# Kernel tuning notes

Hardware: AMD Instinct MI355X
Metric: run time of the kernel (lower is better)

## Reference

```python
import jax, jax.numpy as jnp
import numpy as np

NEG_SLOPE = 0.2


def add_self_loops(edge_index, num_nodes):
    loop = jnp.arange(num_nodes, dtype=edge_index.dtype)
    return jnp.concatenate([edge_index, jnp.stack([loop, loop])], axis=1)


def gat_conv(x, edge_index, W, att_src, att_dst, bias, heads, out_ch, concat):
    # x: [N, F_in]; edge_index: [2, E]; W: [F_in, heads*out_ch]
    # att_src/att_dst: [heads, out_ch]; bias: [heads*out_ch] or [out_ch]
    N = x.shape[0]
    ei = add_self_loops(edge_index, N)
    src, dst = ei[0], ei[1]
    xw = (x @ W).reshape(N, heads, out_ch)          # [N, H, C]
    a_src = jnp.einsum('nhc,hc->nh', xw, att_src)    # [N, H]
    a_dst = jnp.einsum('nhc,hc->nh', xw, att_dst)    # [N, H]
    e = a_src[src] + a_dst[dst]                      # [E', H]
    e = jax.nn.leaky_relu(e, NEG_SLOPE)
    # segment softmax over edges grouped by destination node
    e_max = jax.ops.segment_max(e, dst, num_segments=N)  # [N, H]
    e_exp = jnp.exp(e - e_max[dst])
    denom = jax.ops.segment_sum(e_exp, dst, num_segments=N)  # [N, H]
    alpha = e_exp / denom[dst]                       # [E', H]
    msg = xw[src] * alpha[:, :, None]                # [E', H, C]
    out = jax.ops.segment_sum(msg, dst, num_segments=N)  # [N, H, C]
    if concat:
        out = out.reshape(N, heads * out_ch)
    else:
        out = out.mean(axis=1)
    return out + bias


def setup_inputs() -> dict:
    key = jax.random.key(0)
    ks = jax.random.split(key, 10)
    N, E = 100000, 1600000
    F_in, hid, heads, F_out = 128, 32, 4, 40
    s = 0.1
    x = jax.random.normal(ks[0], (N, F_in), dtype=jnp.float32)
    edge_index = jax.random.randint(ks[1], (2, E), 0, N, dtype=jnp.int64)
    W1 = jax.random.normal(ks[2], (F_in, heads * hid), dtype=jnp.float32) * s
    att_src1 = jax.random.normal(ks[3], (heads, hid), dtype=jnp.float32) * s
    att_dst1 = jax.random.normal(ks[4], (heads, hid), dtype=jnp.float32) * s
    b1 = jax.random.normal(ks[5], (heads * hid,), dtype=jnp.float32) * s
    W2 = jax.random.normal(ks[6], (heads * hid, F_out), dtype=jnp.float32) * s
    att_src2 = jax.random.normal(ks[7], (1, F_out), dtype=jnp.float32) * s
    att_dst2 = jax.random.normal(ks[8], (1, F_out), dtype=jnp.float32) * s
    b2 = jax.random.normal(ks[9], (F_out,), dtype=jnp.float32) * s
    return {"x": x, "edge_index": edge_index, "W1": W1, "att_src1": att_src1,
            "att_dst1": att_dst1, "b1": b1, "W2": W2, "att_src2": att_src2,
            "att_dst2": att_dst2, "b2": b2}


def reference(x, edge_index, W1, att_src1, att_dst1, b1, W2, att_src2, att_dst2, b2):
    h = gat_conv(x, edge_index, W1, att_src1, att_dst1, b1, heads=4, out_ch=32, concat=True)
    h = jax.nn.relu(h)
    out = gat_conv(h, edge_index, W2, att_src2, att_dst2, b2, heads=1, out_ch=40, concat=True)
    return out
```

## Files before the change

### kernel.cpp

```cpp
#include <hip/hip_runtime.h>
#include <hip/hip_bf16.h>

#define NEG_SLOPE 0.2f
#define LOG2E 1.4426950408889634f
#define HWREG_XCC_ID_FULL (((32 - 1) << 11) | (0 << 6) | 20)

typedef _Float16 f16;
typedef f16 f16x8 __attribute__((ext_vector_type(8)));
typedef float f32x4 __attribute__((ext_vector_type(4)));
typedef float fvec4 __attribute__((ext_vector_type(4)));
typedef unsigned uvec4 __attribute__((ext_vector_type(4)));

template <typename T>
__device__ __forceinline__ T ntload(const T* p) { return __builtin_nontemporal_load(p); }
template <typename T>
__device__ __forceinline__ void ntstore(T* p, T v) { __builtin_nontemporal_store(v, p); }

__device__ __forceinline__ float4 ntload4f(const float4* p) {
    fvec4 v = __builtin_nontemporal_load((const fvec4*)p);
    return make_float4(v.x, v.y, v.z, v.w);
}
__device__ __forceinline__ uint4 ntload4u(const uint4* p) {
    uvec4 v = __builtin_nontemporal_load((const uvec4*)p);
    return (uint4){v.x, v.y, v.z, v.w};
}
__device__ __forceinline__ void ntstore4u(uint4* p, uint4 v) {
    uvec4 t = {v.x, v.y, v.z, v.w};
    __builtin_nontemporal_store(t, (uvec4*)p);
}

__device__ __forceinline__ unsigned pack_h2(float a, float b) {
    union { f16 h[2]; unsigned u; } c;
    c.h[0] = (f16)a; c.h[1] = (f16)b;
    return c.u;
}

__global__ void k_init(const int* __restrict__ ei32, int npairs, int* __restrict__ flag,
                       const float* __restrict__ W1, const float* __restrict__ W2,
                       f16* __restrict__ W1t, f16* __restrict__ W2t,
                       uint4* __restrict__ deg_part4, int nzero) {
    const int b = blockIdx.x, t = threadIdx.x;
    if (b == 0) {
        __shared__ int found;
        if (t == 0) found = 0;
        __syncthreads();
        for (int i = t; i < npairs; i += 256) {
            if (ei32[2 * i + 1] != 0) found = 1;
        }
        __syncthreads();
        if (t == 0) *flag = found ? 0 : 1;
    } else if (b <= 88) {
        int o = (b - 1) * 256 + t;
        if (o < 128 * 128) {
            int n = o >> 7, k = o & 127;
            W1t[o] = (f16)W1[k * 128 + n];
        } else {
            int o2 = o - 128 * 128;
            if (o2 < 48 * 128) {
                int n = o2 >> 7, k = o2 & 127;
                W2t[o2] = (f16)(n < 40 ? W2[k * 40 + n] : 0.f);
            }
        }
    } else {
        int idx = (b - 89) * 256 + t;
        if (idx < nzero) deg_part4[idx] = (uint4){0, 0, 0, 0};
    }
}

__global__ void k_degree(const void* __restrict__ ei, const int* __restrict__ flag,
                         int* __restrict__ deg_part, int* __restrict__ rank, int N, int E) {
    int e = blockIdx.x * blockDim.x + threadIdx.x;
    if (e >= E) return;
    int d;
    if (*flag) d = (int)ntload(&((const long long*)ei)[(long long)E + e]);
    else       d = ntload(&((const int*)ei)[E + e]);
    int xcc = (int)(__builtin_amdgcn_s_getreg(HWREG_XCC_ID_FULL) & 7u);
    int lr = atomicAdd(&deg_part[xcc * N + d], 1);
    ntstore(&rank[e], (xcc << 24) | lr);
}

__global__ __launch_bounds__(1024) void k_scan_blk(int* __restrict__ deg_part,
                                                   int* __restrict__ offsets,
                                                   int* __restrict__ blksum, int N) {
    __shared__ int wsums[16];
    const int t = threadIdx.x;
    const int lane = t & 63;
    const int wid = t >> 6;
    int idx = blockIdx.x * 4096 + t * 4;
    int v0 = 0, v1 = 0, v2 = 0, v3 = 0;
    if (((N & 3) == 0) && (idx + 3 < N)) {
        uint4 u[8];
#pragma unroll
        for (int x = 0; x < 8; x++) u[x] = *(uint4*)&deg_part[x * N + idx];
        int p0 = 0, p1 = 0, p2 = 0, p3 = 0;
#pragma unroll
        for (int x = 0; x < 8; x++) {
            uint4 w = u[x];
            u[x] = (uint4){(unsigned)p0, (unsigned)p1, (unsigned)p2, (unsigned)p3};
            p0 += (int)w.x; p1 += (int)w.y; p2 += (int)w.z; p3 += (int)w.w;
        }
#pragma unroll
        for (int x = 0; x < 8; x++) *(uint4*)&deg_part[x * N + idx] = u[x];
        v0 = p0; v1 = p1; v2 = p2; v3 = p3;
    } else if (idx < N) {
        int vv[4] = {0, 0, 0, 0};
        for (int i = 0; i < 4; i++) {
            int d = idx + i;
            if (d >= N) break;
            int p = 0;
#pragma unroll
            for (int x = 0; x < 8; x++) {
                int t0 = deg_part[x * N + d];
                deg_part[x * N + d] = p;
                p += t0;
            }
            vv[i] = p;
        }
        v0 = vv[0]; v1 = vv[1]; v2 = vv[2]; v3 = vv[3];
    }
    int s1 = v0 + v1, s2 = s1 + v2, s3 = s2 + v3;
    int inc = s3;
#pragma unroll
    for (int off = 1; off < 64; off <<= 1) {
        int y = __shfl_up(inc, off);
        if (lane >= off) inc += y;
    }
    if (lane == 63) wsums[wid] = inc;
    __syncthreads();
    if (wid == 0) {
        int v = (lane < 16) ? wsums[lane] : 0;
        int wi = v;
#pragma unroll
        for (int off = 1; off < 16; off <<= 1) {
            int y = __shfl_up(wi, off);
            if (lane >= off) wi += y;
        }
        if (lane < 16) wsums[lane] = wi - v;
        if (lane == 15) blksum[blockIdx.x] = wi;
    }
    __syncthreads();
    int excl = wsums[wid] + (inc - s3);
    if (idx + 0 < N) offsets[idx + 1] = excl + v0;
    if (idx + 1 < N) offsets[idx + 2] = excl + s1;
    if (idx + 2 < N) offsets[idx + 3] = excl + s2;
    if (idx + 3 < N) offsets[idx + 4] = excl + s3;
}

__global__ void k_scan_top(const int* __restrict__ blksum, int* __restrict__ blkoff, int G) {
    int l = threadIdx.x;
    int v = (l < G) ? blksum[l] : 0;
    int inc = v;
#pragma unroll
    for (int off = 1; off < 64; off <<= 1) {
        int y = __shfl_up(inc, off);
        if (l >= off) inc += y;
    }
    if (l < G) blkoff[l] = inc - v;
}

__global__ void k_scan_add(int* __restrict__ offsets, const int* __restrict__ blkoff, int N) {
    int n = blockIdx.x * blockDim.x + threadIdx.x;
    if (n >= N) return;
    offsets[n + 1] += blkoff[n >> 12];
    if (n == 0) offsets[0] = 0;
}

__global__ void k_scatter(const void* __restrict__ ei, const int* __restrict__ flag,
                          const int* __restrict__ offsets, const int* __restrict__ deg_part,
                          const int* __restrict__ rank, int* __restrict__ csr_src,
                          int N, int E) {
    int e = blockIdx.x * blockDim.x + threadIdx.x;
    if (e >= E) return;
    int s, d;
    if (*flag) {
        const long long* p = (const long long*)ei;
        s = (int)ntload(&p[e]);
        d = (int)ntload(&p[(long long)E + e]);
    } else {
        const int* p = (const int*)ei;
        s = ntload(&p[e]);
        d = ntload(&p[E + e]);
    }
    int r = ntload(&rank[e]);
    int xcc = r >> 24;
    int lr = r & 0xFFFFFF;
    ntstore(&csr_src[offsets[d] + deg_part[xcc * N + d] + lr], s);
}

__global__ __launch_bounds__(256) void k_gemm1(const float* __restrict__ X,
                                               const f16* __restrict__ W1t,
                                               const float* __restrict__ as1,
                                               const float* __restrict__ ad1,
                                               f16* __restrict__ Af,
                                               float* __restrict__ aS1,
                                               float* __restrict__ aD1, int N) {
    __shared__ f16 sA[64 * 136];
    __shared__ f16 sB[128 * 136];
    const int t = threadIdx.x;
    const int row0 = blockIdx.x * 64;

    {
        int r = t >> 2, seg = t & 3;
        int row = row0 + r;
        if (row >= N) row = N - 1;
        const float4* xg = (const float4*)(X + (size_t)row * 128 + seg * 32);
        unsigned tmp[16];
#pragma unroll
        for (int j = 0; j < 8; j++) {
            float4 v = ntload4f(&xg[j]);
            tmp[2 * j]     = pack_h2(v.x, v.y);
            tmp[2 * j + 1] = pack_h2(v.z, v.w);
        }
        uint4* dst = (uint4*)&sA[r * 136 + seg * 32];
#pragma unroll
        for (int j = 0; j < 4; j++) dst[j] = ((uint4*)tmp)[j];
        int n = t >> 1, half = (t & 1) * 64;
        const uint4* src = (const uint4*)(W1t + n * 128 + half);
        uint4* dw = (uint4*)&sB[n * 136 + half];
#pragma unroll
        for (int j = 0; j < 8; j++) dw[j] = src[j];
    }
    __syncthreads();

    const int w = t >> 6, lane = t & 63, ln = lane & 15, q = lane >> 4;
    f32x4 acc[8];
#pragma unroll
    for (int c = 0; c < 8; c++) acc[c] = (f32x4){0.f, 0.f, 0.f, 0.f};

#pragma unroll
    for (int ks = 0; ks < 4; ks++) {
        f16x8 a = *(const f16x8*)&sA[(w * 16 + ln) * 136 + ks * 32 + q * 8];
#pragma unroll
        for (int c = 0; c < 8; c++) {
            f16x8 b = *(const f16x8*)&sB[(c * 16 + ln) * 136 + ks * 32 + q * 8];
            acc[c] = __builtin_amdgcn_mfma_f32_16x16x32_f16(a, b, acc[c], 0, 0, 0);
        }
    }

#pragma unroll
    for (int c = 0; c < 8; c++)
#pragma unroll
        for (int reg = 0; reg < 4; reg++) {
            int rg = row0 + w * 16 + q * 4 + reg;
            if (rg < N) ntstore(&Af[(size_t)rg * 128 + c * 16 + ln], (f16)acc[c][reg]);
        }

    float ps[4][4], pd[4][4];
#pragma unroll
    for (int h = 0; h < 4; h++) {
        float as_lo = as1[32 * h + ln], as_hi = as1[32 * h + 16 + ln];
        float ad_lo = ad1[32 * h + ln], ad_hi = ad1[32 * h + 16 + ln];
#pragma unroll
        for (int reg = 0; reg < 4; reg++) {
            ps[h][reg] = acc[2 * h][reg] * as_lo + acc[2 * h + 1][reg] * as_hi;
            pd[h][reg] = acc[2 * h][reg] * ad_lo + acc[2 * h + 1][reg] * ad_hi;
        }
    }
#pragma unroll
    for (int h = 0; h < 4; h++)
#pragma unroll
        for (int reg = 0; reg < 4; reg++)
#pragma unroll
            for (int off = 1; off < 16; off <<= 1) {
                ps[h][reg] += __shfl_xor(ps[h][reg], off);
                pd[h][reg] += __shfl_xor(pd[h][reg], off);
            }
#pragma unroll
    for (int h = 0; h < 4; h++) {
        if (ln == 2 * h) {
#pragma unroll
            for (int reg = 0; reg < 4; reg++) {
                int rg = row0 + w * 16 + q * 4 + reg;
                if (rg < N) aS1[rg * 4 + h] = ps[h][reg] * LOG2E;
            }
        }
        if (ln == 2 * h + 1) {
#pragma unroll
            for (int reg = 0; reg < 4; reg++) {
                int rg = row0 + w * 16 + q * 4 + reg;
                if (rg < N) aD1[rg * 4 + h] = pd[h][reg] * LOG2E;
            }
        }
    }
}

__global__ __launch_bounds__(256) void k_gemm2(const f16* __restrict__ Hf,
                                               const f16* __restrict__ W2t,
                                               const float* __restrict__ as2,
                                               const float* __restrict__ ad2,
                                               f16* __restrict__ X2f,
                                               float* __restrict__ aS2,
                                               float* __restrict__ aD2, int N) {
    __shared__ f16 sA[64 * 136];
    __shared__ f16 sB[48 * 136];
    const int t = threadIdx.x;
    const int row0 = blockIdx.x * 64;
    {
        int r = t >> 2, seg = t & 3;
        int row = row0 + r;
        if (row >= N) row = N - 1;
        const uint4* hg = (const uint4*)(Hf + (size_t)row * 128 + seg * 32);
        uint4* dst = (uint4*)&sA[r * 136 + seg * 32];
#pragma unroll
        for (int j = 0; j < 4; j++) dst[j] = ntload4u(&hg[j]);
        const uint4* wsrc = (const uint4*)W2t;
#pragma unroll
        for (int u = t; u < 768; u += 256) {
            int o = u * 8;
            int n = o >> 7, ko = o & 127;
            *(uint4*)&sB[n * 136 + ko] = wsrc[u];
        }
    }
    __syncthreads();

    const int w = t >> 6, lane = t & 63, ln = lane & 15, q = lane >> 4;
    f32x4 acc[3];
#pragma unroll
    for (int c = 0; c < 3; c++) acc[c] = (f32x4){0.f, 0.f, 0.f, 0.f};

#pragma unroll
    for (int ks = 0; ks < 4; ks++) {
        f16x8 a = *(const f16x8*)&sA[(w * 16 + ln) * 136 + ks * 32 + q * 8];
#pragma unroll
        for (int c = 0; c < 3; c++) {
            f16x8 b = *(const f16x8*)&sB[(c * 16 + ln) * 136 + ks * 32 + q * 8];
            acc[c] = __builtin_amdgcn_mfma_f32_16x16x32_f16(a, b, acc[c], 0, 0, 0);
        }
    }

#pragma unroll
    for (int c = 0; c < 3; c++) {
        int col = c * 16 + ln;
        if (col < 40) {
#pragma unroll
            for (int reg = 0; reg < 4; reg++) {
                int rg = row0 + w * 16 + q * 4 + reg;
                if (rg < N) X2f[(size_t)rg * 64 + col] = (f16)acc[c][reg];
            }
        }
    }

    float ps[4], pd[4];
#pragma unroll
    for (int reg = 0; reg < 4; reg++) { ps[reg] = 0.f; pd[reg] = 0.f; }
#pragma unroll
    for (int c = 0; c < 3; c++) {
        int col = c * 16 + ln;
        float as_ = (col < 40) ? as2[col] : 0.f;
        float ad_ = (col < 40) ? ad2[col] : 0.f;
#pragma unroll
        for (int reg = 0; reg < 4; reg++) {
            ps[reg] = fmaf(acc[c][reg], as_, ps[reg]);
            pd[reg] = fmaf(acc[c][reg], ad_, pd[reg]);
        }
    }
#pragma unroll
    for (int reg = 0; reg < 4; reg++) {
#pragma unroll
        for (int off = 1; off < 16; off <<= 1) {
            ps[reg] += __shfl_xor(ps[reg], off);
            pd[reg] += __shfl_xor(pd[reg], off);
        }
        int rg = row0 + w * 16 + q * 4 + reg;
        if (rg < N) {
            if (ln == 0) aS2[rg] = ps[reg] * LOG2E;
            if (ln == 1) aD2[rg] = pd[reg] * LOG2E;
        }
    }
}

__global__ __launch_bounds__(256) void k_msg1(const int* __restrict__ offsets,
                                              const int* __restrict__ csr_src,
                                              const float* __restrict__ aS,
                                              const float* __restrict__ aD,
                                              const f16* __restrict__ Af,
                                              const float* __restrict__ b1,
                                              f16* __restrict__ Hf, int N) {
    const int lane = threadIdx.x & 63;
    const int n = blockIdx.x * 4 + (threadIdx.x >> 6);
    const bool node_ok = (n < N);
    const int g = lane >> 4;
    const int p = lane & 15;
    const int h = p >> 2;

    int b = 0, e = 0;
    float adh = 0.f;
    if (node_ok) {
        b = offsets[n];
        e = offsets[n + 1];
        adh = aD[n * 4 + h];
    }

    float acc[8];
#pragma unroll
    for (int k = 0; k < 8; k++) acc[k] = 0.f;
    float wsum = 0.f;

    if (node_ok) {
        float xs = aS[n * 4 + h] + adh;
        float ws = __builtin_amdgcn_exp2f(fmaxf(xs, NEG_SLOPE * xs));
        if (g != 0) ws = 0.f;
        const f16x8 hv = *(const f16x8*)(Af + (size_t)n * 128 + p * 8);
#pragma unroll
        for (int k = 0; k < 8; k++) acc[k] = fmaf(ws, (float)hv[k], acc[k]);
        wsum = ws;
    }

    int sreg = 0;
    if (node_ok && e > b) {
        int idx = b + lane;
        if (idx >= e) idx = e - 1;
        sreg = ntload(&csr_src[idx]);
    }

    int i = b;
#pragma unroll 2
    for (; i < e && (i - b) + 4 <= 64; i += 4) {
        int j = i + g;
        bool valid = (j < e);
        int s = __builtin_amdgcn_ds_bpermute((j - b) << 2, sreg);
        if (!valid) s = 0;
        float sv = aS[s * 4 + h];
        const f16x8 hv = *(const f16x8*)(Af + (size_t)s * 128 + p * 8);
        float x = sv + adh;
        float wgt = __builtin_amdgcn_exp2f(fmaxf(x, NEG_SLOPE * x));
        if (!valid) wgt = 0.f;
#pragma unroll
        for (int k = 0; k < 8; k++) acc[k] = fmaf(wgt, (float)hv[k], acc[k]);
        wsum += wgt;
    }
    for (; i < e; i += 4) {
        int j = i + g;
        bool valid = (j < e);
        int jc = valid ? j : (e - 1);
        int s = csr_src[jc];
        if (!valid) s = 0;
        float sv = aS[s * 4 + h];
        const f16x8 hv = *(const f16x8*)(Af + (size_t)s * 128 + p * 8);
        float x = sv + adh;
        float wgt = __builtin_amdgcn_exp2f(fmaxf(x, NEG_SLOPE * x));
        if (!valid) wgt = 0.f;
#pragma unroll
        for (int k = 0; k < 8; k++) acc[k] = fmaf(wgt, (float)hv[k], acc[k]);
        wsum += wgt;
    }

#pragma unroll
    for (int k = 0; k < 8; k++) {
        acc[k] += __shfl_xor(acc[k], 16);
        acc[k] += __shfl_xor(acc[k], 32);
    }
    wsum += __shfl_xor(wsum, 16);
    wsum += __shfl_xor(wsum, 32);

    if (node_ok && g == 0) {
        float inv = __builtin_amdgcn_rcpf(wsum);
        const float4* bb = (const float4*)(b1 + p * 8);
        float4 b0 = bb[0], b4 = bb[1];
        float bv[8] = {b0.x, b0.y, b0.z, b0.w, b4.x, b4.y, b4.z, b4.w};
        union { f16 h8[8]; uint4 u; } o;
#pragma unroll
        for (int k = 0; k < 8; k++) {
            float v = fmaf(acc[k], inv, bv[k]);
            o.h8[k] = (f16)fmaxf(v, 0.f);
        }
        ntstore4u((uint4*)(Hf + (size_t)n * 128 + p * 8), o.u);
    }
}

__global__ __launch_bounds__(256) void k_msg2(const int* __restrict__ offsets,
                                              const int* __restrict__ csr_src,
                                              const float* __restrict__ aS,
                                              const float* __restrict__ aD,
                                              const f16* __restrict__ X2f,
                                              const float* __restrict__ b2,
                                              float* __restrict__ OUT, int N) {
    __shared__ float red[4][60][9];
    const int lane = threadIdx.x & 63;
    const int wv = threadIdx.x >> 6;
    const int n = blockIdx.x * 4 + wv;
    const bool node_ok = (n < N);
    const int g = lane / 5;
    const int p = lane % 5;
    const bool lane_ok = (g < 12);

    int b = 0, e = 0;
    float adh = 0.f;
    if (node_ok) {
        b = offsets[n];
        e = offsets[n + 1];
        adh = aD[n];
    }

    float acc[8];
#pragma unroll
    for (int k = 0; k < 8; k++) acc[k] = 0.f;
    float wsum = 0.f;

    if (node_ok) {
        float xs = aS[n] + adh;
        float ws = __builtin_amdgcn_exp2f(fmaxf(xs, NEG_SLOPE * xs));
        if (!(lane_ok && g == 0)) ws = 0.f;
        const f16x8 hv = *(const f16x8*)(X2f + (size_t)n * 64 + p * 8);
#pragma unroll
        for (int k = 0; k < 8; k++) acc[k] = fmaf(ws, (float)hv[k], acc[k]);
        wsum = ws;
    }

    int sreg = 0;
    if (node_ok && e > b) {
        int idx = b + lane;
        if (idx >= e) idx = e - 1;
        sreg = ntload(&csr_src[idx]);
    }

    int i = b;
    for (; i < e && (i - b) + 12 <= 64; i += 12) {
        int j = i + g;
        bool valid = lane_ok && (j < e);
        int s = __builtin_amdgcn_ds_bpermute(((j - b) & 63) << 2, sreg);
        if (!valid) s = 0;
        float sv = aS[s];
        const f16x8 hv = *(const f16x8*)(X2f + (size_t)s * 64 + p * 8);
        float x = sv + adh;
        float wgt = __builtin_amdgcn_exp2f(fmaxf(x, NEG_SLOPE * x));
        if (!valid) wgt = 0.f;
#pragma unroll
        for (int k = 0; k < 8; k++) acc[k] = fmaf(wgt, (float)hv[k], acc[k]);
        wsum += wgt;
    }
    for (; i < e; i += 12) {
        int j = i + g;
        bool valid = lane_ok && (j < e);
        int jc = (j < e) ? j : (e - 1);
        int s = csr_src[jc];
        if (!valid) s = 0;
        float sv = aS[s];
        const f16x8 hv = *(const f16x8*)(X2f + (size_t)s * 64 + p * 8);
        float x = sv + adh;
        float wgt = __builtin_amdgcn_exp2f(fmaxf(x, NEG_SLOPE * x));
        if (!valid) wgt = 0.f;
#pragma unroll
        for (int k = 0; k < 8; k++) acc[k] = fmaf(wgt, (float)hv[k], acc[k]);
        wsum += wgt;
    }

    if (lane_ok) {
#pragma unroll
        for (int k = 0; k < 8; k++) red[wv][lane][k] = acc[k];
        red[wv][lane][8] = wsum;
    }
    __syncthreads();

    if (node_ok && lane < 40) {
        int pp = lane >> 3, kk = lane & 7;
        float s_ = 0.f, ws_ = 0.f;
#pragma unroll
        for (int gg = 0; gg < 12; gg++) {
            s_  += red[wv][gg * 5 + pp][kk];
            ws_ += red[wv][gg * 5][8];
        }
        float inv = __builtin_amdgcn_rcpf(ws_);
        ntstore(&OUT[(size_t)n * 40 + lane], fmaf(s_, inv, b2[lane]));
    }
}

extern "C" void kernel_launch(void* const* d_in, const int* in_sizes, int n_in,
                              void* d_out, int out_size, void* d_ws, size_t ws_size,
                              hipStream_t stream) {
    const float* x   = (const float*)d_in[0];
    const void*  ei  = d_in[1];
    const float* W1  = (const float*)d_in[2];
    const float* as1 = (const float*)d_in[3];
    const float* ad1 = (const float*)d_in[4];
    const float* b1  = (const float*)d_in[5];
    const float* W2  = (const float*)d_in[6];
    const float* as2 = (const float*)d_in[7];
    const float* ad2 = (const float*)d_in[8];
    const float* b2  = (const float*)d_in[9];
    float* out = (float*)d_out;

    const int N = in_sizes[0] / 128;
    const int E = in_sizes[1] / 2;

    char* w = (char*)d_ws;
    auto alloc = [&](size_t bytes) {
        char* p = w;
        w += (bytes + 15) & ~(size_t)15;
        return p;
    };
    int* flag      = (int*)alloc(16);
    int* offsets   = (int*)alloc((size_t)(N + 1) * 4);
    int* deg_part  = (int*)alloc((size_t)N * 8 * 4);
    int* rank      = (int*)alloc((size_t)E * 4);
    int* csr_src   = (int*)alloc((size_t)E * 4);
    int* blksum    = (int*)alloc(64 * 4);
    int* blkoff    = (int*)alloc(64 * 4);
    float* aS1     = (float*)alloc((size_t)N * 4 * 4);
    float* aD1     = (float*)alloc((size_t)N * 4 * 4);
    float* aS2     = (float*)alloc((size_t)N * 4);
    float* aD2     = (float*)alloc((size_t)N * 4);
    f16* W1t       = (f16*)alloc(128 * 128 * 2);
    f16* W2t       = (f16*)alloc(48 * 128 * 2);
    f16* Af        = (f16*)alloc((size_t)N * 128 * 2);
    f16* X2f       = (f16*)alloc((size_t)N * 64 * 2);
    f16* Hf        = (f16*)alloc((size_t)N * 128 * 2);

    const int nzero = 2 * N;
    k_init<<<89 + (nzero + 255) / 256, 256, 0, stream>>>(
        (const int*)ei, 1024, flag, W1, W2, W1t, W2t, (uint4*)deg_part, nzero);

    k_degree<<<(E + 255) / 256, 256, 0, stream>>>(ei, flag, deg_part, rank, N, E);
    const int G = (N + 4095) / 4096;
    k_scan_blk<<<G, 1024, 0, stream>>>(deg_part, offsets, blksum, N);
    k_scan_top<<<1, 64, 0, stream>>>(blksum, blkoff, G);
    k_scan_add<<<(N + 255) / 256, 256, 0, stream>>>(offsets, blkoff, N);
    k_scatter<<<(E + 255) / 256, 256, 0, stream>>>(ei, flag, offsets, deg_part, rank,
                                                   csr_src, N, E);

    const int gb = (N + 63) / 64;
    k_gemm1<<<gb, 256, 0, stream>>>(x, W1t, as1, ad1, Af, aS1, aD1, N);
    k_msg1<<<(N + 3) / 4, 256, 0, stream>>>(offsets, csr_src, aS1, aD1, Af, b1, Hf, N);

    k_gemm2<<<gb, 256, 0, stream>>>(Hf, W2t, as2, ad2, X2f, aS2, aD2, N);
    k_msg2<<<(N + 3) / 4, 256, 0, stream>>>(offsets, csr_src, aS2, aD2, X2f, b2, out, N);
}
```

Measured before the change: 431.4 us.

## Fuse degree counting into gemm1 launch and drop nontemporal memory hints

```diff
diff --git a/kernel.cpp b/kernel.cpp
--- a/kernel.cpp
+++ b/kernel.cpp
@@ -8,26 +8,6 @@
 typedef _Float16 f16;
 typedef f16 f16x8 __attribute__((ext_vector_type(8)));
 typedef float f32x4 __attribute__((ext_vector_type(4)));
-typedef float fvec4 __attribute__((ext_vector_type(4)));
-typedef unsigned uvec4 __attribute__((ext_vector_type(4)));
-
-template <typename T>
-__device__ __forceinline__ T ntload(const T* p) { return __builtin_nontemporal_load(p); }
-template <typename T>
-__device__ __forceinline__ void ntstore(T* p, T v) { __builtin_nontemporal_store(v, p); }
-
-__device__ __forceinline__ float4 ntload4f(const float4* p) {
-    fvec4 v = __builtin_nontemporal_load((const fvec4*)p);
-    return make_float4(v.x, v.y, v.z, v.w);
-}
-__device__ __forceinline__ uint4 ntload4u(const uint4* p) {
-    uvec4 v = __builtin_nontemporal_load((const uvec4*)p);
-    return (uint4){v.x, v.y, v.z, v.w};
-}
-__device__ __forceinline__ void ntstore4u(uint4* p, uint4 v) {
-    uvec4 t = {v.x, v.y, v.z, v.w};
-    __builtin_nontemporal_store(t, (uvec4*)p);
-}
 
 __device__ __forceinline__ unsigned pack_h2(float a, float b) {
     union { f16 h[2]; unsigned u; } c;
@@ -67,18 +47,6 @@
     }
 }
 
-__global__ void k_degree(const void* __restrict__ ei, const int* __restrict__ flag,
-                         int* __restrict__ deg_part, int* __restrict__ rank, int N, int E) {
-    int e = blockIdx.x * blockDim.x + threadIdx.x;
-    if (e >= E) return;
-    int d;
-    if (*flag) d = (int)ntload(&((const long long*)ei)[(long long)E + e]);
-    else       d = ntload(&((const int*)ei)[E + e]);
-    int xcc = (int)(__builtin_amdgcn_s_getreg(HWREG_XCC_ID_FULL) & 7u);
-    int lr = atomicAdd(&deg_part[xcc * N + d], 1);
-    ntstore(&rank[e], (xcc << 24) | lr);
-}
-
 __global__ __launch_bounds__(1024) void k_scan_blk(int* __restrict__ deg_part,
                                                    int* __restrict__ offsets,
                                                    int* __restrict__ blksum, int N) {
@@ -174,31 +142,53 @@
     int s, d;
     if (*flag) {
         const long long* p = (const long long*)ei;
-        s = (int)ntload(&p[e]);
-        d = (int)ntload(&p[(long long)E + e]);
+        s = (int)p[e];
+        d = (int)p[(long long)E + e];
     } else {
         const int* p = (const int*)ei;
-        s = ntload(&p[e]);
-        d = ntload(&p[E + e]);
-    }
-    int r = ntload(&rank[e]);
+        s = p[e];
+        d = p[E + e];
+    }
+    int r = rank[e];
     int xcc = r >> 24;
     int lr = r & 0xFFFFFF;
-    ntstore(&csr_src[offsets[d] + deg_part[xcc * N + d] + lr], s);
-}
-
-__global__ __launch_bounds__(256) void k_gemm1(const float* __restrict__ X,
-                                               const f16* __restrict__ W1t,
-                                               const float* __restrict__ as1,
-                                               const float* __restrict__ ad1,
-                                               f16* __restrict__ Af,
-                                               float* __restrict__ aS1,
-                                               float* __restrict__ aD1, int N) {
+    csr_src[offsets[d] + deg_part[xcc * N + d] + lr] = s;
+}
+
+__global__ __launch_bounds__(256) void k_gemm1deg(const float* __restrict__ X,
+                                                  const f16* __restrict__ W1t,
+                                                  const float* __restrict__ as1,
+                                                  const float* __restrict__ ad1,
+                                                  f16* __restrict__ Af,
+                                                  float* __restrict__ aS1,
+                                                  float* __restrict__ aD1, int N, int gb,
+                                                  const void* __restrict__ ei,
+                                                  const int* __restrict__ flag,
+                                                  int* __restrict__ deg_part,
+                                                  int* __restrict__ rank, int E) {
     __shared__ f16 sA[64 * 136];
     __shared__ f16 sB[128 * 136];
     const int t = threadIdx.x;
+
+    if (blockIdx.x >= gb) {
+        const int base = (blockIdx.x - gb) * 1024;
+        const int f64 = *flag;
+        const int xcc = (int)(__builtin_amdgcn_s_getreg(HWREG_XCC_ID_FULL) & 7u);
+#pragma unroll
+        for (int k = 0; k < 4; k++) {
+            int e = base + k * 256 + t;
+            if (e < E) {
+                int d;
+                if (f64) d = (int)((const long long*)ei)[(long long)E + e];
+                else     d = ((const int*)ei)[E + e];
+                int lr = atomicAdd(&deg_part[xcc * N + d], 1);
+                rank[e] = (xcc << 24) | lr;
+            }
+        }
+        return;
+    }
+
     const int row0 = blockIdx.x * 64;
-
     {
         int r = t >> 2, seg = t & 3;
         int row = row0 + r;
@@ -207,7 +197,7 @@
         unsigned tmp[16];
 #pragma unroll
         for (int j = 0; j < 8; j++) {
-            float4 v = ntload4f(&xg[j]);
+            float4 v = xg[j];
             tmp[2 * j]     = pack_h2(v.x, v.y);
             tmp[2 * j + 1] = pack_h2(v.z, v.w);
         }
@@ -242,7 +232,7 @@
 #pragma unroll
         for (int reg = 0; reg < 4; reg++) {
             int rg = row0 + w * 16 + q * 4 + reg;
-            if (rg < N) ntstore(&Af[(size_t)rg * 128 + c * 16 + ln], (f16)acc[c][reg]);
+            if (rg < N) Af[(size_t)rg * 128 + c * 16 + ln] = (f16)acc[c][reg];
         }
 
     float ps[4][4], pd[4][4];
@@ -302,7 +292,7 @@
         const uint4* hg = (const uint4*)(Hf + (size_t)row * 128 + seg * 32);
         uint4* dst = (uint4*)&sA[r * 136 + seg * 32];
 #pragma unroll
-        for (int j = 0; j < 4; j++) dst[j] = ntload4u(&hg[j]);
+        for (int j = 0; j < 4; j++) dst[j] = hg[j];
         const uint4* wsrc = (const uint4*)W2t;
 #pragma unroll
         for (int u = t; u < 768; u += 256) {
@@ -410,7 +400,7 @@
     if (node_ok && e > b) {
         int idx = b + lane;
         if (idx >= e) idx = e - 1;
-        sreg = ntload(&csr_src[idx]);
+        sreg = csr_src[idx];
     }
 
     int i = b;
@@ -464,7 +454,7 @@
             float v = fmaf(acc[k], inv, bv[k]);
             o.h8[k] = (f16)fmaxf(v, 0.f);
         }
-        ntstore4u((uint4*)(Hf + (size_t)n * 128 + p * 8), o.u);
+        *(uint4*)(Hf + (size_t)n * 128 + p * 8) = o.u;
     }
 }
 
@@ -511,7 +501,7 @@
     if (node_ok && e > b) {
         int idx = b + lane;
         if (idx >= e) idx = e - 1;
-        sreg = ntload(&csr_src[idx]);
+        sreg = csr_src[idx];
     }
 
     int i = b;
@@ -561,7 +551,7 @@
             ws_ += red[wv][gg * 5][8];
         }
         float inv = __builtin_amdgcn_rcpf(ws_);
-        ntstore(&OUT[(size_t)n * 40 + lane], fmaf(s_, inv, b2[lane]));
+        OUT[(size_t)n * 40 + lane] = fmaf(s_, inv, b2[lane]);
     }
 }
 
@@ -610,7 +600,11 @@
     k_init<<<89 + (nzero + 255) / 256, 256, 0, stream>>>(
         (const int*)ei, 1024, flag, W1, W2, W1t, W2t, (uint4*)deg_part, nzero);
 
-    k_degree<<<(E + 255) / 256, 256, 0, stream>>>(ei, flag, deg_part, rank, N, E);
+    const int gb = (N + 63) / 64;
+    const int degB = (E + 1023) / 1024;
+    k_gemm1deg<<<gb + degB, 256, 0, stream>>>(x, W1t, as1, ad1, Af, aS1, aD1, N, gb,
+                                              ei, flag, deg_part, rank, E);
+
     const int G = (N + 4095) / 4096;
     k_scan_blk<<<G, 1024, 0, stream>>>(deg_part, offsets, blksum, N);
     k_scan_top<<<1, 64, 0, stream>>>(blksum, blkoff, G);
@@ -618,8 +612,6 @@
     k_scatter<<<(E + 255) / 256, 256, 0, stream>>>(ei, flag, offsets, deg_part, rank,
                                                    csr_src, N, E);
 
-    const int gb = (N + 63) / 64;
-    k_gemm1<<<gb, 256, 0, stream>>>(x, W1t, as1, ad1, Af, aS1, aD1, N);
     k_msg1<<<(N + 3) / 4, 256, 0, stream>>>(offsets, csr_src, aS1, aD1, Af, b1, Hf, N);
 
     k_gemm2<<<gb, 256, 0, stream>>>(Hf, W2t, as2, ad2, X2f, aS2, aD2, N);
```

After: 391.3 us. 1.1x faster.
